# Performance work log

Hardware: AMD Instinct MI355X
Metric: run time of the kernel (lower is better)

Reference implementation:

```python
import jax, jax.numpy as jnp
import numpy as np

BS, L, D = 16, 256, 512
H, DQ, DV, DFF, KSZ = 8, 64, 64, 2048, 3


def _ln(x, g, b, eps=1e-5):
    mu = jnp.mean(x, -1, keepdims=True)
    var = jnp.mean((x - mu) ** 2, -1, keepdims=True)
    return (x - mu) / jnp.sqrt(var + eps) * g + b


def _conv(x, w):
    # x: [bs, 1, d] (NCW), w: [1, 1, k], same padding for odd k, no bias
    pad = (w.shape[-1] - 1) // 2
    return jax.lax.conv_general_dilated(x, w, (1,), [(pad, pad)], dimension_numbers=('NCH', 'OIH', 'NCH'))


def setup_inputs() -> dict:
    key = jax.random.key(0)
    ks = jax.random.split(key, 12)
    s = lambda k, shape, sc: jax.random.normal(k, shape, jnp.float32) * sc
    w0 = 0.02
    return {
        'inp': jax.random.normal(ks[0], (BS, L, D), jnp.float32),
        'conv1_w': s(ks[1], (1, 1, KSZ), 0.3),
        'conv2_w': s(ks[2], (1, 1, KSZ), 0.3),
        'ctx_wq': s(ks[3], (D, H * DQ), w0),
        'ctx_wk': s(ks[4], (D, H * DQ), w0),
        'ctx_fc': s(ks[5], (H * DV, D), w0),
        'glb_wq': s(ks[6], (D, H * DQ), w0),
        'glb_wk': s(ks[7], (D, H * DQ), w0),
        'glb_fc': s(ks[8], (H * DV, D), w0),
        'ln1_g': jnp.ones(D), 'ln1_b': jnp.zeros(D),
        'ln2_g': jnp.ones(D), 'ln2_b': jnp.zeros(D),
        'ln3_g': jnp.ones(D), 'ln3_b': jnp.zeros(D),
        'mlp_w1': s(ks[9], (D, DFF), w0), 'mlp_b1': jnp.zeros(DFF),
        'mlp_w2': s(ks[10], (DFF, D), w0), 'mlp_b2': jnp.zeros(D),
    }


def reference(inp, conv1_w, conv2_w, ctx_wq, ctx_wk, ctx_fc,
              glb_wq, glb_wk, glb_fc, ln1_g, ln1_b, ln2_g, ln2_b,
              ln3_g, ln3_b, mlp_w1, mlp_b1, mlp_w2, mlp_b2):
    bs, seqlen, d = inp.shape
    scale = 1.0 / jnp.sqrt(jnp.float32(DQ))
    # Global K/V are step-invariant: hoist out of the recurrence.
    # NOTE: original module (faithfully) projects V with W_Q, not W_V.
    Kg = (inp @ glb_wk).reshape(bs, seqlen, H, DQ).transpose(0, 2, 1, 3)  # [b,h,L,dq]
    Vg = (inp @ glb_wq).reshape(bs, seqlen, H, DV).transpose(0, 2, 1, 3)  # [b,h,L,dv]

    def step(hn, x_i):
        # hn: [bs,1,d] recurrent state, x_i: [bs,d] current token
        x = x_i[:, None, :]                                   # [bs,1,d]
        res = x
        xc = _conv(x, conv1_w)                                # [bs,1,d]
        # context cross-attn: Q=hn, K=xc, V=xc (via W_Q, as in source)
        Qc = (hn @ ctx_wq).reshape(bs, 1, H, DQ).transpose(0, 2, 1, 3)
        Kc = (xc @ ctx_wk).reshape(bs, 1, H, DQ).transpose(0, 2, 1, 3)
        Vc = (xc @ ctx_wq).reshape(bs, 1, H, DV).transpose(0, 2, 1, 3)
        sc = jnp.einsum('bhqd,bhkd->bhqk', Qc, Kc) * scale    # [b,h,1,1]
        ac = jax.nn.softmax(sc, axis=-1)
        ctx = jnp.einsum('bhqk,bhkd->bhqd', ac, Vc)
        ctx = ctx.transpose(0, 2, 1, 3).reshape(bs, 1, H * DV) @ ctx_fc
        x = _ln(ctx + res, ln1_g, ln1_b)
        res = x
        x2 = _conv(x, conv2_w)
        # global cross-attn: Q=x2, K/V from full input (hoisted)
        Qg = (x2 @ glb_wq).reshape(bs, 1, H, DQ).transpose(0, 2, 1, 3)
        sg = jnp.einsum('bhqd,bhkd->bhqk', Qg, Kg) * scale    # [b,h,1,L]
        h = jnp.einsum('bhqk,bhkd->bhqd', jax.nn.softmax(sg, axis=-1), Vg)
        h = h.transpose(0, 2, 1, 3).reshape(bs, 1, H * DV) @ glb_fc  # [bs,1,d]
        x = _ln(h + res, ln2_g, ln2_b)
        y = jax.nn.gelu(x @ mlp_w1 + mlp_b1, approximate=False) @ mlp_w2 + mlp_b2
        y = _ln(y + x, ln3_g, ln3_b)
        return h, y[:, 0, :]

    hn0 = inp[:, 0:1, :]
    hn, ys = jax.lax.scan(step, hn0, jnp.swapaxes(inp, 0, 1))  # ys: [L,bs,d]
    output = jnp.swapaxes(ys, 0, 1)                            # [bs,L,d]
    return output, hn
```

## Files before the change

kernel.cpp:

```cpp
#include <hip/hip_runtime.h>
#include <math.h>

#define NBS 16
#define NL 256
#define ND 512
#define NH 8
#define NDFF 2048
#define NT (NBS*NL)

typedef unsigned short u16;
typedef unsigned int   u32;
typedef __attribute__((ext_vector_type(8))) short bf16x8;
typedef __attribute__((ext_vector_type(4))) float f32x4;

__device__ __forceinline__ u16 f2b(float f){
  u32 u = __float_as_uint(f);
  u32 r = u + 0x7FFFu + ((u >> 16) & 1u);
  return (u16)(r >> 16);
}
__device__ __forceinline__ float blo(u32 u){ return __uint_as_float(u << 16); }
__device__ __forceinline__ float bhi(u32 u){ return __uint_as_float(u & 0xFFFF0000u); }
__device__ __forceinline__ u32 pk2(float a, float b){ return (u32)f2b(a) | ((u32)f2b(b) << 16); }

__device__ __forceinline__ void gl16(const void* g, void* l){
  __builtin_amdgcn_global_load_lds((const __attribute__((address_space(1))) void*)g,
                                   (__attribute__((address_space(3))) void*)l, 16, 0, 0);
}
__device__ __forceinline__ float gelu_f(float x){ return 0.5f*x*(1.f+erff(x*0.70710678118654752f)); }

__device__ inline void tr_tile(const float* __restrict__ src, u16* __restrict__ dst,
                               int K, int N, int ntk, int tb, float* Tsh){
  int tk = tb % ntk, tn = tb / ntk;
  int t = threadIdx.x;
  int r = t >> 2, q = t & 3;
  const float* s = src + (size_t)(tk*64 + r)*N + tn*64 + q*16;
  #pragma unroll
  for (int u2 = 0; u2 < 4; u2++){
    float4 v = *(const float4*)(s + u2*4);
    Tsh[r*65 + q*16 + u2*4 + 0] = v.x;
    Tsh[r*65 + q*16 + u2*4 + 1] = v.y;
    Tsh[r*65 + q*16 + u2*4 + 2] = v.z;
    Tsh[r*65 + q*16 + u2*4 + 3] = v.w;
  }
  __syncthreads();
  int n = t >> 2, kq = t & 3;
  u16* d = dst + (size_t)(tn*64 + n)*K + tk*64 + kq*16;
  u32 u[8];
  #pragma unroll
  for (int j = 0; j < 8; j++){
    u32 lo = f2b(Tsh[(kq*16 + 2*j    )*65 + n]);
    u32 hi = f2b(Tsh[(kq*16 + 2*j + 1)*65 + n]);
    u[j] = lo | (hi << 16);
  }
  ((uint4*)d)[0] = make_uint4(u[0],u[1],u[2],u[3]);
  ((uint4*)d)[1] = make_uint4(u[4],u[5],u[6],u[7]);
}

__global__ __launch_bounds__(256) void pack_k(
    const float* __restrict__ inp,
    const float* __restrict__ ctx_wq, const float* __restrict__ ctx_fc,
    const float* __restrict__ glb_wq, const float* __restrict__ glb_wk,
    const float* __restrict__ glb_fc,
    const float* __restrict__ w1, const float* __restrict__ w2,
    const float* __restrict__ c1w,
    u16* wk_t, u16* wq_t, u16* cfc_t, u16* gfc_t, u16* cwq_bf,
    u16* w1_t, u16* w2_t, u16* inp_bf, u16* xc_bf)
{
  __shared__ float Tsh[64*65];
  int bx = blockIdx.x, t = threadIdx.x;
  if (bx < 256){
    int m = bx >> 6, tb = bx & 63;
    const float* s; u16* d;
    if      (m == 0){ s = glb_wk; d = wk_t; }
    else if (m == 1){ s = glb_wq; d = wq_t; }
    else if (m == 2){ s = ctx_fc; d = cfc_t; }
    else            { s = glb_fc; d = gfc_t; }
    tr_tile(s, d, 512, 512, 8, tb, Tsh);
  } else if (bx < 512){
    tr_tile(w1, w1_t, 512, 2048, 8, bx - 256, Tsh);
  } else if (bx < 768){
    tr_tile(w2, w2_t, 2048, 512, 32, bx - 512, Tsh);
  } else if (bx < 1792){
    size_t i0 = (size_t)(bx - 768)*2048 + (size_t)t*8;
    float4 v0 = *(const float4*)(inp + i0);
    float4 v1 = *(const float4*)(inp + i0 + 4);
    uint4 o;
    o.x = pk2(v0.x, v0.y); o.y = pk2(v0.z, v0.w);
    o.z = pk2(v1.x, v1.y); o.w = pk2(v1.z, v1.w);
    *(uint4*)(inp_bf + i0) = o;
  } else if (bx < 2816){
    size_t i0 = (size_t)(bx - 1792)*2048 + (size_t)t*8;
    float w0 = c1w[0], w1v = c1w[1], w2v = c1w[2];
    u32 u[4];
    #pragma unroll
    for (int j = 0; j < 8; j += 2){
      float f[2];
      #pragma unroll
      for (int s2 = 0; s2 < 2; s2++){
        size_t i = i0 + j + s2; int d = (int)(i & (ND-1));
        float xm = d        ? inp[i-1] : 0.f;
        float x0 = inp[i];
        float xp = (d<ND-1) ? inp[i+1] : 0.f;
        f[s2] = w0*xm + w1v*x0 + w2v*xp;
      }
      u[j>>1] = pk2(f[0], f[1]);
    }
    *(uint4*)(xc_bf + i0) = make_uint4(u[0],u[1],u[2],u[3]);
  } else {
    size_t i0 = (size_t)(bx - 2816)*2048 + (size_t)t*8;
    float4 v0 = *(const float4*)(ctx_wq + i0);
    float4 v1 = *(const float4*)(ctx_wq + i0 + 4);
    uint4 o;
    o.x = pk2(v0.x, v0.y); o.y = pk2(v0.z, v0.w);
    o.z = pk2(v1.x, v1.y); o.w = pk2(v1.z, v1.w);
    *(uint4*)(cwq_bf + i0) = o;
  }
}

template<int TM,int BIAS,int ACT>
__device__ __forceinline__ void gemm2p_core(const u16* __restrict__ A,
    const u16* __restrict__ Bt, const float* __restrict__ bias,
    void* __restrict__ Cb, int N, int K, int lda, int ldb, int outm,
    u16* sm, int row0, int col0)
{
  constexpr int MF = TM/32;
  const int tid = threadIdx.x;
  const int w = tid >> 6, l = tid & 63;
  const int wr = w >> 1, wc = w & 1;
  const int l15 = l & 15, lk = (l >> 4)*16;
  const int srow = tid >> 3;
  const int scol = (((tid & 7)*16) ^ ((srow & 7) << 4)) >> 1;
  const u16* pa = A  + (size_t)(row0 + srow)*lda + scol;
  const u16* pb = Bt + (size_t)(col0 + srow)*ldb + scol;
  char* lA = (char*)sm + (tid & ~63)*16;
  char* lB = (char*)sm + TM*128 + (tid & ~63)*16;

  f32x4 acc[MF][2] = {};
  const int nt = K >> 6;

  for (int t = 0; t < nt; ++t){
    __syncthreads();
    #pragma unroll
    for (int i = 0; i < MF; i++)
      gl16(pa + t*64 + (size_t)(i*32)*lda, lA + i*4096);
    gl16(pb + t*64,                  lB);
    gl16(pb + t*64 + (size_t)32*ldb, lB + 4096);
    __syncthreads();
    const char* bA = (const char*)sm;
    const char* bB = (const char*)sm + TM*128;
    #pragma unroll
    for (int ks = 0; ks < 2; ks++){
      bf16x8 af[MF], bv[2];
      #pragma unroll
      for (int m = 0; m < MF; m++){
        int r = wr*(TM/2) + m*16 + l15;
        af[m] = *(const bf16x8*)(bA + r*128 + ((ks*64 + lk) ^ ((r & 7) << 4)));
      }
      #pragma unroll
      for (int n = 0; n < 2; n++){
        int r = wc*32 + n*16 + l15;
        bv[n] = *(const bf16x8*)(bB + r*128 + ((ks*64 + lk) ^ ((r & 7) << 4)));
      }
      #pragma unroll
      for (int m = 0; m < MF; m++)
        #pragma unroll
        for (int n = 0; n < 2; n++)
          acc[m][n] = __builtin_amdgcn_mfma_f32_16x16x32_bf16(af[m], bv[n], acc[m][n], 0, 0, 0);
    }
  }

  #pragma unroll
  for (int m = 0; m < MF; m++){
    #pragma unroll
    for (int n = 0; n < 2; n++){
      int col = col0 + wc*32 + n*16 + l15;
      int rowb = row0 + wr*(TM/2) + m*16 + (l >> 4)*4;
      if (outm == 2){
        uint2 o;
        o.x = pk2(acc[m][n][0], acc[m][n][1]);
        o.y = pk2(acc[m][n][2], acc[m][n][3]);
        *(uint2*)((u16*)Cb + (size_t)(rowb >> 8)*131072 + (size_t)col*256 + (rowb & 255)) = o;
      } else if (outm == 0){
        #pragma unroll
        for (int rr = 0; rr < 4; rr++)
          ((float*)Cb)[(size_t)(rowb + rr)*N + col] = acc[m][n][rr];
      } else {
        #pragma unroll
        for (int rr = 0; rr < 4; rr++){
          float v = acc[m][n][rr];
          if (BIAS) v += bias[col];
          if (ACT)  v = gelu_f(v);
          ((u16*)Cb)[(size_t)(rowb + rr)*N + col] = f2b(v);
        }
      }
    }
  }
}

template<int TM,int BIAS,int ACT>
__global__ __launch_bounds__(256) void gemm_k(const u16* __restrict__ A,
                                              const u16* __restrict__ Bt,
                                              const float* __restrict__ bias,
                                              void* __restrict__ Cb, int N, int K)
{
  __shared__ u16 sm[TM*64 + 4096];
  gemm2p_core<TM,BIAS,ACT>(A, Bt, bias, Cb, N, K, K, K, 1, sm,
                           blockIdx.y*TM, blockIdx.x*64);
}

__global__ __launch_bounds__(256) void gemm3_k(
    const u16* __restrict__ A0, const u16* __restrict__ B0, u16* __restrict__ C0,
    const u16* __restrict__ A1, const u16* __restrict__ B1, u16* __restrict__ C1,
    const u16* __restrict__ A2, const u16* __restrict__ B2, u16* __restrict__ C2)
{
  __shared__ u16 sm[128*64 + 4096];
  const u16 *A, *Bt; u16* Cb; int outm = 1;
  if (blockIdx.z == 0){ A = A0; Bt = B0; Cb = C0; }
  else if (blockIdx.z == 1){ A = A1; Bt = B1; Cb = C1; outm = 2; }
  else { A = A2; Bt = B2; Cb = C2; }
  gemm2p_core<128,0,0>(A, Bt, nullptr, Cb, 512, 512, 512, 512, outm, sm,
                       blockIdx.y*128, blockIdx.x*64);
}

__global__ __launch_bounds__(256) void gemm_w2sk(const u16* __restrict__ G,
                                                 const u16* __restrict__ w2t,
                                                 float* __restrict__ P)
{
  __shared__ u16 sm[64*64 + 4096];
  const int z = blockIdx.z;
  gemm2p_core<64,0,0>(G + z*1024, w2t + z*1024, nullptr,
                      (void*)(P + (size_t)z*NT*512), 512, 1024, 2048, 2048, 0,
                      sm, blockIdx.y*64, blockIdx.x*64);
}

__global__ __launch_bounds__(256) void qattn_k(const u16* __restrict__ X2,
                                               const u16* __restrict__ Wq,
                                               const u16* __restrict__ Kg,
                                               const u16* __restrict__ Vt,
                                               u16* __restrict__ O)
{
  __shared__ u16 sm[40960];
  const int h = blockIdx.x, ty = blockIdx.y;
  const int b = ty >> 2, bh = b*8 + h;
  const int tid = threadIdx.x;
  const int w = tid >> 6, l = tid & 63;
  const int l15 = l & 15, lg = l >> 4;
  const int wr = w >> 1, wc = w & 1;
  const int lk = lg*16;

  {
    const int vrow = tid >> 5;
    const int vcb  = (tid*16) & 511;
    const int scolV = (vcb ^ ((vrow & 7) << 4)) >> 1;
    const u16* pv = Vt + (size_t)bh*16384 + (size_t)vrow*256 + scolV;
    char* lV = (char*)sm + 40960 + (tid & ~63)*16;
    #pragma unroll
    for (int c = 0; c < 8; c++)
      gl16(pv + (size_t)(c*8)*256, lV + c*4096);
  }

  const int srow = tid >> 3;
  const int scol = (((tid & 7)*16) ^ ((srow & 7) << 4)) >> 1;
  const u16* pa = X2 + (size_t)(ty*64 + srow)*512 + scol;
  const u16* pb = Wq + (size_t)(h*64  + srow)*512 + scol;
  char* lS = (char*)sm + (tid & ~63)*16;

  auto QSTG = [&](int buf, int kt){
    char* a = lS + buf*8192;
    char* bq = lS + 16384 + buf*8192;
    gl16(pa + kt,              a);
    gl16(pa + kt + 32*512,     a + 4096);
    gl16(pb + kt,              bq);
    gl16(pb + kt + 32*512,     bq + 4096);
  };

  f32x4 qacc[2][2] = {};
  QSTG(0, 0);
  __syncthreads();
  for (int t = 0; t < 8; ++t){
    if (t < 7) QSTG((t+1) & 1, (t+1)*64);
    const char* bA = (const char*)sm + (t&1)*8192;
    const char* bB = (const char*)sm + 16384 + (t&1)*8192;
    #pragma unroll
    for (int ks = 0; ks < 2; ks++){
      bf16x8 af[2], bv[2];
      #pragma unroll
      for (int m = 0; m < 2; m++){
        int r = wr*32 + m*16 + l15;
        af[m] = *(const bf16x8*)(bA + r*128 + ((ks*64 + lk) ^ ((r & 7) << 4)));
      }
      #pragma unroll
      for (int n = 0; n < 2; n++){
        int r = wc*32 + n*16 + l15;
        bv[n] = *(const bf16x8*)(bB + r*128 + ((ks*64 + lk) ^ ((r & 7) << 4)));
      }
      #pragma unroll
      for (int m = 0; m < 2; m++)
        #pragma unroll
        for (int n = 0; n < 2; n++)
          qacc[m][n] = __builtin_amdgcn_mfma_f32_16x16x32_bf16(af[m], bv[n], qacc[m][n], 0, 0, 0);
    }
    __syncthreads();
  }

  {
    const u16* pk = Kg + (size_t)(b*256 + srow)*512 + h*64 + scol;
    char* lK = (char*)sm + (tid & ~63)*16;
    #pragma unroll
    for (int c = 0; c < 8; c++)
      gl16(pk + (size_t)(c*32)*512, lK + c*4096);
  }
  #pragma unroll
  for (int m = 0; m < 2; m++)
    #pragma unroll
    for (int n = 0; n < 2; n++)
      #pragma unroll
      for (int rr = 0; rr < 4; rr++){
        int row = wr*32 + m*16 + (l >> 4)*4 + rr;
        int col = wc*32 + n*16 + l15;
        *(u16*)((char*)sm + 32768 + row*128 + ((col*2) ^ ((row & 7) << 4))) = f2b(qacc[m][n][rr]);
      }
  __syncthreads();

  const int qt0 = b*256 + (ty & 3)*64 + w*16;
  bf16x8 aq[2];
  #pragma unroll
  for (int ks = 0; ks < 2; ks++){
    int qr = w*16 + l15;
    aq[ks] = *(const bf16x8*)((char*)sm + 32768 + qr*128 + ((ks*64 + lk) ^ ((qr & 7) << 4)));
  }
  char* Pw = (char*)sm + 73728 + w*2048;

  f32x4 oacc[4] = {};
  float rsum[4] = {0.f, 0.f, 0.f, 0.f};

  #pragma unroll
  for (int c = 0; c < 4; c++){
    f32x4 sacc[4] = {};
    #pragma unroll
    for (int n = 0; n < 4; n++){
      int r = c*64 + n*16 + l15;
      #pragma unroll
      for (int ks = 0; ks < 2; ks++){
        bf16x8 bk = *(const bf16x8*)((const char*)sm + r*128 + ((ks*64 + lk) ^ ((r & 7) << 4)));
        sacc[n] = __builtin_amdgcn_mfma_f32_16x16x32_bf16(aq[ks], bk, sacc[n], 0, 0, 0);
      }
    }
    #pragma unroll
    for (int n = 0; n < 4; n++){
      #pragma unroll
      for (int rr = 0; rr < 4; rr++){
        float p = __expf(sacc[n][rr]*0.125f);
        rsum[rr] += p;
        int q = lg*4 + rr, key = n*16 + l15;
        *(u16*)(Pw + ((q*128 + key*2) ^ ((q & 7) << 4))) = f2b(p);
      }
    }
    bf16x8 ap[2];
    #pragma unroll
    for (int ks2 = 0; ks2 < 2; ks2++)
      ap[ks2] = *(const bf16x8*)(Pw + l15*128 + ((ks2*64 + lk) ^ ((l15 & 7) << 4)));
    #pragma unroll
    for (int n = 0; n < 4; n++){
      int r = n*16 + l15;
      #pragma unroll
      for (int ks2 = 0; ks2 < 2; ks2++){
        bf16x8 bvv = *(const bf16x8*)((const char*)sm + 40960 + r*512 +
                                      ((c*128 + ks2*64 + lk) ^ ((r & 7) << 4)));
        oacc[n] = __builtin_amdgcn_mfma_f32_16x16x32_bf16(ap[ks2], bvv, oacc[n], 0, 0, 0);
      }
    }
  }

  #pragma unroll
  for (int m = 1; m < 16; m <<= 1){
    #pragma unroll
    for (int rr = 0; rr < 4; rr++) rsum[rr] += __shfl_xor(rsum[rr], m);
  }
  #pragma unroll
  for (int n = 0; n < 4; n++){
    int d = h*64 + n*16 + l15;
    #pragma unroll
    for (int rr = 0; rr < 4; rr++){
      int t = qt0 + lg*4 + rr;
      O[(size_t)t*ND + d] = f2b(oacc[n][rr]/rsum[rr]);
    }
  }
}

template<int MODE>
__global__ __launch_bounds__(256) void ln_k(const void* __restrict__ aptr,
                                            const void* __restrict__ bptr,
                                            const float* __restrict__ g,
                                            const float* __restrict__ be,
                                            const float* __restrict__ cw,
                                            const float* __restrict__ a2,
                                            const float* __restrict__ bias2,
                                            u16* __restrict__ obf,
                                            u16* __restrict__ convbf,
                                            float* __restrict__ of32,
                                            float* __restrict__ hnout)
{
  __shared__ float row[512];
  __shared__ float red[10];
  const int r0 = blockIdx.x, tid = threadIdx.x;
  const size_t base = (size_t)r0*ND;
  const int d = tid*2;
  float v0, v1;
  if (MODE == 3){
    float2 p0 = *(const float2*)((const float*)aptr + base + d);
    float2 p1 = *(const float2*)(a2 + base + d);
    u32 bv = *(const u32*)((const u16*)bptr + base + d);
    v0 = p0.x + p1.x + bias2[d]   + blo(bv);
    v1 = p0.y + p1.y + bias2[d+1] + bhi(bv);
  } else {
    u32 av = *(const u32*)((const u16*)aptr + base + d);
    v0 = blo(av); v1 = bhi(av);
    if (MODE == 1 && (r0 & 255) == 255){
      hnout[(size_t)(r0 >> 8)*512 + d]     = v0;
      hnout[(size_t)(r0 >> 8)*512 + d + 1] = v1;
    }
    if (MODE == 0){
      float2 bv = *(const float2*)((const float*)bptr + base + d);
      v0 += bv.x; v1 += bv.y;
    } else {
      u32 bv = *(const u32*)((const u16*)bptr + base + d);
      v0 += blo(bv); v1 += bhi(bv);
    }
  }
  float s = v0+v1, ss = v0*v0+v1*v1;
  #pragma unroll
  for (int m = 1; m < 64; m <<= 1){ s += __shfl_xor(s, m); ss += __shfl_xor(ss, m); }
  int wv = tid >> 6;
  if ((tid & 63) == 0){ red[wv] = s; red[4+wv] = ss; }
  __syncthreads();
  if (tid == 0){
    float S = red[0]+red[1]+red[2]+red[3];
    float SS = red[4]+red[5]+red[6]+red[7];
    float mu = S*(1.f/ND);
    float var = SS*(1.f/ND) - mu*mu;
    red[8] = mu; red[9] = rsqrtf(var + 1e-5f);
  }
  __syncthreads();
  float mu = red[8], rsd = red[9];
  float o0 = (v0-mu)*rsd*g[d]   + be[d];
  float o1 = (v1-mu)*rsd*g[d+1] + be[d+1];
  if (MODE == 3){
    *(float2*)(of32 + base + d) = make_float2(o0, o1);
  } else {
    *(u32*)(obf + base + d) = pk2(o0, o1);
    if (MODE == 0){
      row[d] = o0; row[d+1] = o1;
      __syncthreads();
      float w0 = cw[0], w1v = cw[1], w2v = cw[2];
      float xm = d ? row[d-1] : 0.f;
      float xp2 = (d+2 < 512) ? row[d+2] : 0.f;
      float c0 = w0*xm + w1v*o0 + w2v*o1;
      float c1 = w0*o0 + w1v*o1 + w2v*xp2;
      *(u32*)(convbf + base + d) = pk2(c0, c1);
    }
  }
}

extern "C" void kernel_launch(void* const* d_in, const int* in_sizes, int n_in,
                              void* d_out, int out_size, void* d_ws, size_t ws_size,
                              hipStream_t stream) {
  const float* inp     = (const float*)d_in[0];
  const float* conv1_w = (const float*)d_in[1];
  const float* conv2_w = (const float*)d_in[2];
  const float* ctx_wq  = (const float*)d_in[3];
  const float* ctx_fc  = (const float*)d_in[5];
  const float* glb_wq  = (const float*)d_in[6];
  const float* glb_wk  = (const float*)d_in[7];
  const float* glb_fc  = (const float*)d_in[8];
  const float* ln1_g = (const float*)d_in[9],  *ln1_b = (const float*)d_in[10];
  const float* ln2_g = (const float*)d_in[11], *ln2_b = (const float*)d_in[12];
  const float* ln3_g = (const float*)d_in[13], *ln3_b = (const float*)d_in[14];
  const float* mlp_w1 = (const float*)d_in[15], *mlp_b1 = (const float*)d_in[16];
  const float* mlp_w2 = (const float*)d_in[17], *mlp_b2 = (const float*)d_in[18];
  float* out = (float*)d_out;
  float* hn  = out + (size_t)NT*ND;

  u16* wk_t   = (u16*)d_ws;
  u16* wq_t   = wk_t   + 262144;
  u16* cfc_t  = wq_t   + 262144;
  u16* gfc_t  = cfc_t  + 262144;
  u16* cwq_bf = gfc_t  + 262144;
  u16* Wc_t   = cwq_bf + 262144;
  u16* w1_t   = Wc_t   + 262144;
  u16* w2_t   = w1_t   + 1048576;
  u16* inp_bf = w2_t   + 1048576;
  u16* Abf    = inp_bf + 2097152;
  u16* Bbf    = Abf    + 2097152;
  u16* Cbf    = Bbf    + 2097152;
  u16* Kg     = Cbf    + 2097152;
  u16* Vt     = Kg     + 2097152;
  u16* X1bf   = Vt     + 2097152;
  u16* X3bf   = X1bf   + 2097152;
  u16* Gbf    = X3bf   + 2097152;
  float* Pf   = (float*)(Gbf + 8388608);

  pack_k<<<2944, 256, 0, stream>>>(inp, ctx_wq, ctx_fc, glb_wq, glb_wk, glb_fc,
                                   mlp_w1, mlp_w2, conv1_w,
                                   wk_t, wq_t, cfc_t, gfc_t, cwq_bf, w1_t, w2_t,
                                   inp_bf, Abf);
  gemm_k<64,0,0><<<dim3(8,8),256,0,stream>>>(cfc_t, cwq_bf, nullptr, Wc_t, 512, 512);
  gemm3_k<<<dim3(8,32,3),256,0,stream>>>(inp_bf, wk_t, Kg,
                                         inp_bf, wq_t, Vt,
                                         Abf,    Wc_t, Cbf);
  ln_k<0><<<NT,256,0,stream>>>(Cbf, inp, ln1_g, ln1_b, conv2_w, nullptr, nullptr,
                               X1bf, Abf, nullptr, nullptr);
  qattn_k<<<dim3(8,64),256,0,stream>>>(Abf, wq_t, Kg, Vt, Bbf);
  gemm_k<64,0,0><<<dim3(8,64),256,0,stream>>>(Bbf, gfc_t, nullptr, Cbf, 512, 512);
  ln_k<1><<<NT,256,0,stream>>>(Cbf, X1bf, ln2_g, ln2_b, nullptr, nullptr, nullptr,
                               X3bf, nullptr, nullptr, hn);
  gemm_k<128,1,1><<<dim3(32,32),256,0,stream>>>(X3bf, w1_t, mlp_b1, Gbf, 2048, 512);
  gemm_w2sk<<<dim3(8,64,2),256,0,stream>>>(Gbf, w2_t, Pf);
  ln_k<3><<<NT,256,0,stream>>>(Pf, X3bf, ln3_g, ln3_b, nullptr, Pf + (size_t)NT*512,
                               mlp_b2, nullptr, nullptr, out, nullptr);
}
```

Measured before the change: 113.7 us.

## Double-buffer GEMM LDS tiles and enlarge MLP GEMM tiles

```diff
diff --git a/kernel.cpp b/kernel.cpp
--- a/kernel.cpp
+++ b/kernel.cpp
@@ -117,13 +117,14 @@
   }
 }
 
-template<int TM,int BIAS,int ACT>
-__device__ __forceinline__ void gemm2p_core(const u16* __restrict__ A,
+template<int TM,int TN,int BIAS,int ACT>
+__device__ __forceinline__ void gemm_core(const u16* __restrict__ A,
     const u16* __restrict__ Bt, const float* __restrict__ bias,
     void* __restrict__ Cb, int N, int K, int lda, int ldb, int outm,
     u16* sm, int row0, int col0)
 {
-  constexpr int MF = TM/32;
+  constexpr int MF = TM/32, NF = TN/32;
+  constexpr int ABUF = TM*128, BBUF = TN*128;
   const int tid = threadIdx.x;
   const int w = tid >> 6, l = tid & 63;
   const int wr = w >> 1, wc = w & 1;
@@ -132,48 +133,56 @@
   const int scol = (((tid & 7)*16) ^ ((srow & 7) << 4)) >> 1;
   const u16* pa = A  + (size_t)(row0 + srow)*lda + scol;
   const u16* pb = Bt + (size_t)(col0 + srow)*ldb + scol;
-  char* lA = (char*)sm + (tid & ~63)*16;
-  char* lB = (char*)sm + TM*128 + (tid & ~63)*16;
-
-  f32x4 acc[MF][2] = {};
+  char* lA0 = (char*)sm + (tid & ~63)*16;
+  char* lB0 = (char*)sm + 2*ABUF + (tid & ~63)*16;
+
+  f32x4 acc[MF][NF] = {};
   const int nt = K >> 6;
 
+  auto STAGE = [&](int buf, int kt){
+    char* a = lA0 + buf*ABUF;
+    char* b = lB0 + buf*BBUF;
+    #pragma unroll
+    for (int i = 0; i < MF; i++)
+      gl16(pa + kt + (size_t)(i*32)*lda, a + i*4096);
+    #pragma unroll
+    for (int i = 0; i < NF; i++)
+      gl16(pb + kt + (size_t)(i*32)*ldb, b + i*4096);
+  };
+
+  STAGE(0, 0);
+  __syncthreads();
   for (int t = 0; t < nt; ++t){
-    __syncthreads();
-    #pragma unroll
-    for (int i = 0; i < MF; i++)
-      gl16(pa + t*64 + (size_t)(i*32)*lda, lA + i*4096);
-    gl16(pb + t*64,                  lB);
-    gl16(pb + t*64 + (size_t)32*ldb, lB + 4096);
-    __syncthreads();
-    const char* bA = (const char*)sm;
-    const char* bB = (const char*)sm + TM*128;
+    if (t + 1 < nt) STAGE((t+1) & 1, (t+1)*64);
+    const char* bA = (const char*)sm + (t&1)*ABUF;
+    const char* bB = (const char*)sm + 2*ABUF + (t&1)*BBUF;
     #pragma unroll
     for (int ks = 0; ks < 2; ks++){
-      bf16x8 af[MF], bv[2];
+      bf16x8 af[MF], bv[NF];
       #pragma unroll
       for (int m = 0; m < MF; m++){
         int r = wr*(TM/2) + m*16 + l15;
         af[m] = *(const bf16x8*)(bA + r*128 + ((ks*64 + lk) ^ ((r & 7) << 4)));
       }
       #pragma unroll
-      for (int n = 0; n < 2; n++){
-        int r = wc*32 + n*16 + l15;
+      for (int n = 0; n < NF; n++){
+        int r = wc*(TN/2) + n*16 + l15;
         bv[n] = *(const bf16x8*)(bB + r*128 + ((ks*64 + lk) ^ ((r & 7) << 4)));
       }
       #pragma unroll
       for (int m = 0; m < MF; m++)
         #pragma unroll
-        for (int n = 0; n < 2; n++)
+        for (int n = 0; n < NF; n++)
           acc[m][n] = __builtin_amdgcn_mfma_f32_16x16x32_bf16(af[m], bv[n], acc[m][n], 0, 0, 0);
     }
+    __syncthreads();
   }
 
   #pragma unroll
   for (int m = 0; m < MF; m++){
     #pragma unroll
-    for (int n = 0; n < 2; n++){
-      int col = col0 + wc*32 + n*16 + l15;
+    for (int n = 0; n < NF; n++){
+      int col = col0 + wc*(TN/2) + n*16 + l15;
       int rowb = row0 + wr*(TM/2) + m*16 + (l >> 4)*4;
       if (outm == 2){
         uint2 o;
@@ -197,15 +206,15 @@
   }
 }
 
-template<int TM,int BIAS,int ACT>
+template<int TM,int TN,int BIAS,int ACT>
 __global__ __launch_bounds__(256) void gemm_k(const u16* __restrict__ A,
                                               const u16* __restrict__ Bt,
                                               const float* __restrict__ bias,
                                               void* __restrict__ Cb, int N, int K)
 {
-  __shared__ u16 sm[TM*64 + 4096];
-  gemm2p_core<TM,BIAS,ACT>(A, Bt, bias, Cb, N, K, K, K, 1, sm,
-                           blockIdx.y*TM, blockIdx.x*64);
+  __shared__ u16 sm[(TM+TN)*128];
+  gemm_core<TM,TN,BIAS,ACT>(A, Bt, bias, Cb, N, K, K, K, 1, sm,
+                            blockIdx.y*TM, blockIdx.x*TN);
 }
 
 __global__ __launch_bounds__(256) void gemm3_k(
@@ -213,24 +222,24 @@
     const u16* __restrict__ A1, const u16* __restrict__ B1, u16* __restrict__ C1,
     const u16* __restrict__ A2, const u16* __restrict__ B2, u16* __restrict__ C2)
 {
-  __shared__ u16 sm[128*64 + 4096];
+  __shared__ u16 sm[(128+64)*128];
   const u16 *A, *Bt; u16* Cb; int outm = 1;
   if (blockIdx.z == 0){ A = A0; Bt = B0; Cb = C0; }
   else if (blockIdx.z == 1){ A = A1; Bt = B1; Cb = C1; outm = 2; }
   else { A = A2; Bt = B2; Cb = C2; }
-  gemm2p_core<128,0,0>(A, Bt, nullptr, Cb, 512, 512, 512, 512, outm, sm,
-                       blockIdx.y*128, blockIdx.x*64);
+  gemm_core<128,64,0,0>(A, Bt, nullptr, Cb, 512, 512, 512, 512, outm, sm,
+                        blockIdx.y*128, blockIdx.x*64);
 }
 
 __global__ __launch_bounds__(256) void gemm_w2sk(const u16* __restrict__ G,
                                                  const u16* __restrict__ w2t,
                                                  float* __restrict__ P)
 {
-  __shared__ u16 sm[64*64 + 4096];
+  __shared__ u16 sm[(128+64)*128];
   const int z = blockIdx.z;
-  gemm2p_core<64,0,0>(G + z*1024, w2t + z*1024, nullptr,
-                      (void*)(P + (size_t)z*NT*512), 512, 1024, 2048, 2048, 0,
-                      sm, blockIdx.y*64, blockIdx.x*64);
+  gemm_core<128,64,0,0>(G + z*1024, w2t + z*1024, nullptr,
+                        (void*)(P + (size_t)z*NT*512), 512, 1024, 2048, 2048, 0,
+                        sm, blockIdx.y*128, blockIdx.x*64);
 }
 
 __global__ __launch_bounds__(256) void qattn_k(const u16* __restrict__ X2,
@@ -504,18 +513,18 @@
                                    mlp_w1, mlp_w2, conv1_w,
                                    wk_t, wq_t, cfc_t, gfc_t, cwq_bf, w1_t, w2_t,
                                    inp_bf, Abf);
-  gemm_k<64,0,0><<<dim3(8,8),256,0,stream>>>(cfc_t, cwq_bf, nullptr, Wc_t, 512, 512);
+  gemm_k<64,64,0,0><<<dim3(8,8),256,0,stream>>>(cfc_t, cwq_bf, nullptr, Wc_t, 512, 512);
   gemm3_k<<<dim3(8,32,3),256,0,stream>>>(inp_bf, wk_t, Kg,
                                          inp_bf, wq_t, Vt,
                                          Abf,    Wc_t, Cbf);
   ln_k<0><<<NT,256,0,stream>>>(Cbf, inp, ln1_g, ln1_b, conv2_w, nullptr, nullptr,
                                X1bf, Abf, nullptr, nullptr);
   qattn_k<<<dim3(8,64),256,0,stream>>>(Abf, wq_t, Kg, Vt, Bbf);
-  gemm_k<64,0,0><<<dim3(8,64),256,0,stream>>>(Bbf, gfc_t, nullptr, Cbf, 512, 512);
+  gemm_k<64,64,0,0><<<dim3(8,64),256,0,stream>>>(Bbf, gfc_t, nullptr, Cbf, 512, 512);
   ln_k<1><<<NT,256,0,stream>>>(Cbf, X1bf, ln2_g, ln2_b, nullptr, nullptr, nullptr,
                                X3bf, nullptr, nullptr, hn);
-  gemm_k<128,1,1><<<dim3(32,32),256,0,stream>>>(X3bf, w1_t, mlp_b1, Gbf, 2048, 512);
-  gemm_w2sk<<<dim3(8,64,2),256,0,stream>>>(Gbf, w2_t, Pf);
+  gemm_k<128,128,1,1><<<dim3(16,32),256,0,stream>>>(X3bf, w1_t, mlp_b1, Gbf, 2048, 512);
+  gemm_w2sk<<<dim3(8,32,2),256,0,stream>>>(Gbf, w2_t, Pf);
   ln_k<3><<<NT,256,0,stream>>>(Pf, X3bf, ln3_g, ln3_b, nullptr, Pf + (size_t)NT*512,
                                mlp_b2, nullptr, nullptr, out, nullptr);
 }
```

After: 112.3 us. No clear change (-1.2%).
